# Kernel optimization log

Measured on AMD Instinct MI355X. Metric: run time of the kernel, lower is better.

The kernel has to match this reference:

```python
import jax, jax.numpy as jnp
import numpy as np

HIDDEN = 1024
FFN = 4 * HIDDEN
NUM_EXPERTS = 8
TOP_K = 2
B, S = 4, 2048


def setup_inputs() -> dict:
    key = jax.random.key(0)
    ks = jax.random.split(key, 7)
    scale = 0.02
    return {
        "x": jax.random.normal(ks[0], (B, S, HIDDEN), dtype=jnp.float32),
        "gate_w": jax.random.normal(ks[1], (HIDDEN, NUM_EXPERTS), dtype=jnp.float32) * scale,
        "gate_b": jnp.zeros((NUM_EXPERTS,), dtype=jnp.float32),
        "w1": jax.random.normal(ks[2], (NUM_EXPERTS, HIDDEN, FFN), dtype=jnp.float32) * scale,
        "b1": jnp.zeros((NUM_EXPERTS, FFN), dtype=jnp.float32),
        "w2": jax.random.normal(ks[3], (NUM_EXPERTS, FFN, HIDDEN), dtype=jnp.float32) * scale,
        "b2": jnp.zeros((NUM_EXPERTS, HIDDEN), dtype=jnp.float32),
    }


def reference(x, gate_w, gate_b, w1, b1, w2, b2):
    b, s, h = x.shape
    xt = x.reshape(b * s, h)  # [T, H]
    # gate: Linear + softmax
    probs = jax.nn.softmax(xt @ gate_w + gate_b, axis=-1)  # [T, E]
    _, idx = jax.lax.top_k(probs, TOP_K)  # [T, K] int32
    # one-hot over top-k -> boolean per-expert mask (matches original one_hot.sum>0)
    one_hot = jax.nn.one_hot(idx, NUM_EXPERTS, dtype=xt.dtype)  # [T, K, E]
    mask = (one_hot.sum(axis=1) > 0).astype(xt.dtype)  # [T, E]
    # every expert MLP applied to all tokens (dense equivalent of gather-MLP-scatter),
    # then masked combine: output[t] = sum_e mask[t,e] * MLP_e(x[t])
    h1 = jax.nn.relu(jnp.einsum('th,ehf->etf', xt, w1) + b1[:, None, :])  # [E, T, F]
    out_e = jnp.einsum('etf,efh->eth', h1, w2) + b2[:, None, :]  # [E, T, H]
    out = jnp.einsum('eth,te->th', out_e, mask)  # [T, H]
    return out.reshape(b, s, h)
```

## Files before the change

kernel.cpp:

```cpp
#include <hip/hip_runtime.h>

typedef __bf16 bf16_t;
typedef bf16_t bf16x8 __attribute__((ext_vector_type(8)));
typedef bf16_t bf16x4 __attribute__((ext_vector_type(4)));
typedef float floatx4 __attribute__((ext_vector_type(4)));

#define T_TOKENS 8192
#define HIDDEN 1024
#define FFN 4096
#define NE 8
#define PAIRS 16384
#define NTILES 136
#define BK 64

#define GLD16(gp, lp) __builtin_amdgcn_global_load_lds( \
    (const __attribute__((address_space(1))) void*)(gp), \
    (__attribute__((address_space(3))) void*)(lp), 16, 0, 0)

__global__ __launch_bounds__(256) void gate_kernel(
    const float* __restrict__ x, const float* __restrict__ gw,
    const float* __restrict__ gb, unsigned* __restrict__ top2,
    int* __restrict__ counts, bf16_t* __restrict__ xb)
{
    const int lane = threadIdx.x & 63;
    const int wid  = threadIdx.x >> 6;
    const int t    = blockIdx.x * 4 + wid;
    const float4* xr = (const float4*)(x + (size_t)t * HIDDEN);
    bf16_t* xo = xb + (size_t)t * HIDDEN;

    float s[NE];
#pragma unroll
    for (int e = 0; e < NE; ++e) s[e] = 0.f;
#pragma unroll
    for (int ii = 0; ii < 4; ++ii) {
        const int i = ii * 64 + lane;
        float4 v = xr[i];
        bf16x4 b;
        b[0] = (bf16_t)v.x; b[1] = (bf16_t)v.y; b[2] = (bf16_t)v.z; b[3] = (bf16_t)v.w;
        *(bf16x4*)(xo + i * 4) = b;
        const float* g = gw + (size_t)i * 32;
#pragma unroll
        for (int j = 0; j < 4; ++j) {
            const float xv = (&v.x)[j];
#pragma unroll
            for (int e = 0; e < NE; ++e) s[e] += xv * g[j * 8 + e];
        }
    }
#pragma unroll
    for (int e = 0; e < NE; ++e) {
#pragma unroll
        for (int off = 32; off > 0; off >>= 1) s[e] += __shfl_xor(s[e], off, 64);
    }
    if (lane == 0) {
        float v1 = -1e30f, v2 = -1e30f;
        int i1 = 0, i2 = 0;
#pragma unroll
        for (int e = 0; e < NE; ++e) {
            float v = s[e] + gb[e];
            if (v > v1)      { v2 = v1; i2 = i1; v1 = v; i1 = e; }
            else if (v > v2) { v2 = v;  i2 = e; }
        }
        top2[t] = (unsigned)(i1 | (i2 << 4));
        atomicAdd(&counts[i1], 1);
        atomicAdd(&counts[i2], 1);
    }
}

__global__ void offsets_kernel(const int* __restrict__ counts,
                               int* __restrict__ offs,
                               int* __restrict__ tinfo)
{
    int acc = 0, nt = 0;
    for (int e = 0; e < NE; ++e) {
        offs[e] = acc;
        int n = counts[e];
        for (int r = 0; r < n; r += 128) tinfo[nt++] = e | ((r >> 7) << 4);
        acc += n;
    }
    for (; nt < NTILES; ++nt) tinfo[nt] = (65535 << 4);
}

__global__ __launch_bounds__(256) void scatter_kernel(
    const unsigned* __restrict__ top2, const int* __restrict__ offs,
    int* __restrict__ fill, unsigned short* __restrict__ tok16)
{
    const int t = blockIdx.x * 256 + threadIdx.x;
    const unsigned v = top2[t];
    const int e1 = v & 15, e2 = (v >> 4) & 15;
    tok16[offs[e1] + atomicAdd(&fill[e1], 1)] = (unsigned short)t;
    tok16[offs[e2] + atomicAdd(&fill[e2], 1)] = (unsigned short)t;
}

__global__ __launch_bounds__(256) void wtrans_kernel(
    const float* __restrict__ in, bf16_t* __restrict__ out, int R, int C)
{
    __shared__ bf16_t L[64][68];
    const int e  = blockIdx.z;
    const int r0 = blockIdx.y * 64;
    const int c0 = blockIdx.x * 64;
    const float* ip = in + ((size_t)e * R + r0) * C + c0;
    bf16_t* op = out + ((size_t)e * C + c0) * R + r0;
    const int tid = threadIdx.x;
    const int lr = tid >> 4, lc4 = tid & 15;
#pragma unroll
    for (int p = 0; p < 4; ++p) {
        int r = p * 16 + lr;
        float4 v = *(const float4*)(ip + (size_t)r * C + lc4 * 4);
        bf16x4 b;
        b[0] = (bf16_t)v.x; b[1] = (bf16_t)v.y; b[2] = (bf16_t)v.z; b[3] = (bf16_t)v.w;
        *(bf16x4*)&L[r][lc4 * 4] = b;
    }
    __syncthreads();
#pragma unroll
    for (int p = 0; p < 4; ++p) {
        int c  = p * 16 + lr;
        int rr = lc4 * 4;
        bf16x4 b;
        b[0] = L[rr + 0][c]; b[1] = L[rr + 1][c];
        b[2] = L[rr + 2][c]; b[3] = L[rr + 3][c];
        *(bf16x4*)(op + (size_t)c * R + rr) = b;
    }
}

__global__ __launch_bounds__(256, 3) void moe_gemm1(
    const bf16_t* __restrict__ xb, const bf16_t* __restrict__ w1t,
    const float* __restrict__ b1, const int* __restrict__ counts,
    const int* __restrict__ offs, const unsigned short* __restrict__ tok16,
    const int* __restrict__ tinfo, bf16_t* __restrict__ h1)
{
    const int nx = gridDim.x;
    const int hw = blockIdx.y * nx + blockIdx.x;
    const int chunk = (nx * gridDim.y) >> 3;
    const int l  = (hw & 7) * chunk + (hw >> 3);
    const int bx = l % nx;
    const int by = l / nx;

    const int info = tinfo[by];
    const int e    = info & 15;
    const int row0 = (info >> 4) << 7;
    const int n_e  = counts[e];
    if (row0 >= n_e) return;
    const int seg   = offs[e];
    const int fcol0 = bx * 128;

    __shared__ bf16_t S[128 * 128];
    bf16_t* As = S;
    bf16_t* Bs = S + 128 * BK;

    const int tid  = threadIdx.x;
    const int wid  = tid >> 6, lane = tid & 63;
    const int wm   = wid & 1,  wn   = wid >> 1;
    const int quad = lane >> 4, lrow = lane & 15;

    const bf16_t* pA[4]; const bf16_t* pB[4];
#pragma unroll
    for (int q = 0; q < 4; ++q) {
        int slot = q * 256 + tid;
        int arow = slot >> 3, ko = slot & 7;
        int kos  = ko ^ (arow & 7);
        int ridx = row0 + arow; if (ridx > n_e - 1) ridx = n_e - 1;
        pA[q] = xb + (size_t)tok16[seg + ridx] * HIDDEN + kos * 8;
        pB[q] = w1t + ((size_t)e * FFN + fcol0 + arow) * HIDDEN + kos * 8;
    }

    floatx4 acc[4][4];
#pragma unroll
    for (int i = 0; i < 4; ++i)
#pragma unroll
        for (int j = 0; j < 4; ++j) acc[i][j] = (floatx4){0.f, 0.f, 0.f, 0.f};

    for (int k0 = 0; k0 < HIDDEN; k0 += BK) {
#pragma unroll
        for (int q = 0; q < 4; ++q) {
            GLD16(pA[q], As + (q * 256 + wid * 64) * 8);
            GLD16(pB[q], Bs + (q * 256 + wid * 64) * 8);
            pA[q] += BK; pB[q] += BK;
        }
        __syncthreads();
#pragma unroll
        for (int h = 0; h < 2; ++h) {
            bf16x8 af[4], bfr[4];
#pragma unroll
            for (int mi = 0; mi < 4; ++mi) {
                int r = wm * 64 + mi * 16 + lrow;
                int g = (h * 4 + quad) ^ (r & 7);
                af[mi] = *(const bf16x8*)&As[(r << 6) + (g << 3)];
            }
#pragma unroll
            for (int ni = 0; ni < 4; ++ni) {
                int r = wn * 64 + ni * 16 + lrow;
                int g = (h * 4 + quad) ^ (r & 7);
                bfr[ni] = *(const bf16x8*)&Bs[(r << 6) + (g << 3)];
            }
#pragma unroll
            for (int mi = 0; mi < 4; ++mi)
#pragma unroll
                for (int ni = 0; ni < 4; ++ni)
                    acc[mi][ni] = __builtin_amdgcn_mfma_f32_16x16x32_bf16(
                        af[mi], bfr[ni], acc[mi][ni], 0, 0, 0);
        }
        __syncthreads();
    }

#pragma unroll
    for (int ni = 0; ni < 4; ++ni) {
        const int col = wn * 64 + ni * 16 + lrow;
        const float bias = b1[(size_t)e * FFN + fcol0 + col];
#pragma unroll
        for (int mi = 0; mi < 4; ++mi)
#pragma unroll
            for (int r = 0; r < 4; ++r) {
                int row = wm * 64 + mi * 16 + quad * 4 + r;
                float v = acc[mi][ni][r] + bias;
                v = v > 0.f ? v : 0.f;
                S[row * 128 + col] = (bf16_t)v;
            }
    }
    __syncthreads();
#pragma unroll
    for (int i = 0; i < 8; ++i) {
        int g16 = i * 256 + tid;
        int row = g16 >> 4;
        int ce  = (g16 & 15) * 8;
        if (row0 + row < n_e)
            *(bf16x8*)(h1 + (size_t)(seg + row0 + row) * FFN + fcol0 + ce) =
                *(const bf16x8*)&S[row * 128 + ce];
    }
}

__global__ __launch_bounds__(256, 3) void moe_gemm2(
    const bf16_t* __restrict__ h1, const bf16_t* __restrict__ w2t,
    const float* __restrict__ b2, const int* __restrict__ counts,
    const int* __restrict__ offs, const unsigned short* __restrict__ tok16,
    const int* __restrict__ tinfo, float* __restrict__ out)
{
    const int nx = gridDim.x;
    const int hw = blockIdx.y * nx + blockIdx.x;
    const int chunk = (nx * gridDim.y) >> 3;
    const int l  = (hw & 7) * chunk + (hw >> 3);
    const int bx = l % nx;
    const int by = l / nx;

    const int info = tinfo[by];
    const int e    = info & 15;
    const int row0 = (info >> 4) << 7;
    const int n_e  = counts[e];
    if (row0 >= n_e) return;
    const int seg   = offs[e];
    const int hcol0 = bx * 128;

    __shared__ bf16_t As[128 * BK];
    __shared__ bf16_t Bs[128 * BK];

    const int tid  = threadIdx.x;
    const int wid  = tid >> 6, lane = tid & 63;
    const int wm   = wid & 1,  wn   = wid >> 1;
    const int quad = lane >> 4, lrow = lane & 15;

    const bf16_t* pA[4]; const bf16_t* pB[4];
#pragma unroll
    for (int q = 0; q < 4; ++q) {
        int slot = q * 256 + tid;
        int arow = slot >> 3, ko = slot & 7;
        int kos  = ko ^ (arow & 7);
        int ridx = row0 + arow; if (ridx > n_e - 1) ridx = n_e - 1;
        pA[q] = h1 + (size_t)(seg + ridx) * FFN + kos * 8;
        pB[q] = w2t + ((size_t)e * HIDDEN + hcol0 + arow) * FFN + kos * 8;
    }

    floatx4 acc[4][4];
#pragma unroll
    for (int i = 0; i < 4; ++i)
#pragma unroll
        for (int j = 0; j < 4; ++j) acc[i][j] = (floatx4){0.f, 0.f, 0.f, 0.f};

    for (int k0 = 0; k0 < FFN; k0 += BK) {
#pragma unroll
        for (int q = 0; q < 4; ++q) {
            GLD16(pA[q], As + (q * 256 + wid * 64) * 8);
            GLD16(pB[q], Bs + (q * 256 + wid * 64) * 8);
            pA[q] += BK; pB[q] += BK;
        }
        __syncthreads();
#pragma unroll
        for (int h = 0; h < 2; ++h) {
            bf16x8 af[4], bfr[4];
#pragma unroll
            for (int mi = 0; mi < 4; ++mi) {
                int r = wm * 64 + mi * 16 + lrow;
                int g = (h * 4 + quad) ^ (r & 7);
                af[mi] = *(const bf16x8*)&As[(r << 6) + (g << 3)];
            }
#pragma unroll
            for (int ni = 0; ni < 4; ++ni) {
                int r = wn * 64 + ni * 16 + lrow;
                int g = (h * 4 + quad) ^ (r & 7);
                bfr[ni] = *(const bf16x8*)&Bs[(r << 6) + (g << 3)];
            }
#pragma unroll
            for (int mi = 0; mi < 4; ++mi)
#pragma unroll
                for (int ni = 0; ni < 4; ++ni)
                    acc[mi][ni] = __builtin_amdgcn_mfma_f32_16x16x32_bf16(
                        af[mi], bfr[ni], acc[mi][ni], 0, 0, 0);
        }
        __syncthreads();
    }

    int tokr[4][4];
#pragma unroll
    for (int mi = 0; mi < 4; ++mi)
#pragma unroll
        for (int r = 0; r < 4; ++r) {
            int row = wm * 64 + mi * 16 + quad * 4 + r;
            tokr[mi][r] = (row0 + row < n_e) ? (int)tok16[seg + row0 + row] : -1;
        }
#pragma unroll
    for (int ni = 0; ni < 4; ++ni) {
        const int col = wn * 64 + ni * 16 + lrow;
        const float bias = b2[(size_t)e * HIDDEN + hcol0 + col];
#pragma unroll
        for (int mi = 0; mi < 4; ++mi)
#pragma unroll
            for (int r = 0; r < 4; ++r) {
                if (tokr[mi][r] >= 0)
                    atomicAdd(out + (size_t)tokr[mi][r] * HIDDEN + hcol0 + col,
                              acc[mi][ni][r] + bias);
            }
    }
}

extern "C" void kernel_launch(void* const* d_in, const int* in_sizes, int n_in,
                              void* d_out, int out_size, void* d_ws, size_t ws_size,
                              hipStream_t stream)
{
    const float* x      = (const float*)d_in[0];
    const float* gate_w = (const float*)d_in[1];
    const float* gate_b = (const float*)d_in[2];
    const float* w1     = (const float*)d_in[3];
    const float* b1     = (const float*)d_in[4];
    const float* w2     = (const float*)d_in[5];
    const float* b2     = (const float*)d_in[6];
    float* out = (float*)d_out;

    char* ws = (char*)d_ws;
    int*      counts = (int*)(ws + 0);
    int*      fill   = (int*)(ws + 32);
    int*      offs   = (int*)(ws + 64);
    int*      tinfo  = (int*)(ws + 96);
    unsigned* top2   = (unsigned*)(ws + 640);
    unsigned short* tok16 = (unsigned short*)(ws + 640 + 32768);
    const size_t o_base = 98560;

    const size_t sz_xb  = (size_t)T_TOKENS * HIDDEN * 2;
    const size_t sz_w1t = (size_t)NE * FFN * HIDDEN * 2;
    const size_t sz_w2t = (size_t)NE * HIDDEN * FFN * 2;
    const size_t sz_h1  = (size_t)PAIRS * FFN * 2;
    const size_t need = o_base + sz_xb + sz_w1t + sz_w2t + sz_h1;
    if (ws_size < need) return;

    bf16_t* xb  = (bf16_t*)(ws + o_base);
    bf16_t* w1t = (bf16_t*)(ws + o_base + sz_xb);
    bf16_t* w2t = (bf16_t*)(ws + o_base + sz_xb + sz_w1t);
    bf16_t* h1  = (bf16_t*)(ws + o_base + sz_xb + sz_w1t + sz_w2t);

    hipMemsetAsync(ws, 0, 96, stream);
    hipMemsetAsync(out, 0, (size_t)T_TOKENS * HIDDEN * sizeof(float), stream);

    gate_kernel<<<T_TOKENS / 4, 256, 0, stream>>>(x, gate_w, gate_b, top2, counts, xb);
    offsets_kernel<<<1, 1, 0, stream>>>(counts, offs, tinfo);
    scatter_kernel<<<T_TOKENS / 256, 256, 0, stream>>>(top2, offs, fill, tok16);

    wtrans_kernel<<<dim3(FFN / 64, HIDDEN / 64, NE), 256, 0, stream>>>(w1, w1t, HIDDEN, FFN);
    wtrans_kernel<<<dim3(HIDDEN / 64, FFN / 64, NE), 256, 0, stream>>>(w2, w2t, FFN, HIDDEN);

    moe_gemm1<<<dim3(FFN / 128, NTILES), 256, 0, stream>>>(
        xb, w1t, b1, counts, offs, tok16, tinfo, h1);
    moe_gemm2<<<dim3(HIDDEN / 128, NTILES), 256, 0, stream>>>(
        h1, w2t, b2, counts, offs, tok16, tinfo, out);
}
```

Measured before the change: 1.013 ms.

## Double-buffer LDS tiles in MoE GEMMs with async prefetch overlap

Both expert GEMM kernels now use two LDS stages so that the next K-tile's global-to-LDS loads are issued before computing on the current tile, with explicit vmcnt waits and raw barriers instead of full syncthreads. MFMA sections are wrapped in s_setprio to favor math waves. The goal is to hide global memory latency behind the matrix math. LDS use doubles to 64KB per block and occupancy bounds drop from 3 to 2 blocks per CU, which could reduce latency hiding across blocks.

After: 1.033 ms. Within noise of the previous version (+2.0%).

```diff
diff --git a/kernel.cpp b/kernel.cpp
--- a/kernel.cpp
+++ b/kernel.cpp
@@ -16,6 +16,15 @@
 #define GLD16(gp, lp) __builtin_amdgcn_global_load_lds( \
     (const __attribute__((address_space(1))) void*)(gp), \
     (__attribute__((address_space(3))) void*)(lp), 16, 0, 0)
+
+#define STAGE8(DA, DB) do { \
+    _Pragma("unroll") \
+    for (int q = 0; q < 4; ++q) { \
+        GLD16(pA[q], (DA) + (q * 256 + wid * 64) * 8); \
+        GLD16(pB[q], (DB) + (q * 256 + wid * 64) * 8); \
+        pA[q] += BK; pB[q] += BK; \
+    } \
+} while (0)
 
 __global__ __launch_bounds__(256) void gate_kernel(
     const float* __restrict__ x, const float* __restrict__ gw,
@@ -122,7 +131,7 @@
     }
 }
 
-__global__ __launch_bounds__(256, 3) void moe_gemm1(
+__global__ __launch_bounds__(256, 2) void moe_gemm1(
     const bf16_t* __restrict__ xb, const bf16_t* __restrict__ w1t,
     const float* __restrict__ b1, const int* __restrict__ counts,
     const int* __restrict__ offs, const unsigned short* __restrict__ tok16,
@@ -143,9 +152,11 @@
     const int seg   = offs[e];
     const int fcol0 = bx * 128;
 
-    __shared__ bf16_t S[128 * 128];
-    bf16_t* As = S;
-    bf16_t* Bs = S + 128 * BK;
+    __shared__ bf16_t S[4 * 128 * BK];
+    bf16_t* As0 = S;
+    bf16_t* Bs0 = S + 128 * BK;
+    bf16_t* As1 = S + 2 * 128 * BK;
+    bf16_t* Bs1 = S + 3 * 128 * BK;
 
     const int tid  = threadIdx.x;
     const int wid  = tid >> 6, lane = tid & 63;
@@ -169,14 +180,7 @@
 #pragma unroll
         for (int j = 0; j < 4; ++j) acc[i][j] = (floatx4){0.f, 0.f, 0.f, 0.f};
 
-    for (int k0 = 0; k0 < HIDDEN; k0 += BK) {
-#pragma unroll
-        for (int q = 0; q < 4; ++q) {
-            GLD16(pA[q], As + (q * 256 + wid * 64) * 8);
-            GLD16(pB[q], Bs + (q * 256 + wid * 64) * 8);
-            pA[q] += BK; pB[q] += BK;
-        }
-        __syncthreads();
+    auto compute = [&](const bf16_t* AS, const bf16_t* BS) {
 #pragma unroll
         for (int h = 0; h < 2; ++h) {
             bf16x8 af[4], bfr[4];
@@ -184,23 +188,46 @@
             for (int mi = 0; mi < 4; ++mi) {
                 int r = wm * 64 + mi * 16 + lrow;
                 int g = (h * 4 + quad) ^ (r & 7);
-                af[mi] = *(const bf16x8*)&As[(r << 6) + (g << 3)];
+                af[mi] = *(const bf16x8*)&AS[(r << 6) + (g << 3)];
             }
 #pragma unroll
             for (int ni = 0; ni < 4; ++ni) {
                 int r = wn * 64 + ni * 16 + lrow;
                 int g = (h * 4 + quad) ^ (r & 7);
-                bfr[ni] = *(const bf16x8*)&Bs[(r << 6) + (g << 3)];
-            }
+                bfr[ni] = *(const bf16x8*)&BS[(r << 6) + (g << 3)];
+            }
+            __builtin_amdgcn_s_setprio(1);
 #pragma unroll
             for (int mi = 0; mi < 4; ++mi)
 #pragma unroll
                 for (int ni = 0; ni < 4; ++ni)
                     acc[mi][ni] = __builtin_amdgcn_mfma_f32_16x16x32_bf16(
                         af[mi], bfr[ni], acc[mi][ni], 0, 0, 0);
+            __builtin_amdgcn_s_setprio(0);
         }
-        __syncthreads();
-    }
+    };
+
+    STAGE8(As0, Bs0);
+    bf16_t* curA = As0; bf16_t* curB = Bs0;
+    bf16_t* nxtA = As1; bf16_t* nxtB = Bs1;
+
+    const int NK = HIDDEN / BK;
+#pragma unroll 2
+    for (int kt = 1; kt < NK; ++kt) {
+        STAGE8(nxtA, nxtB);
+        asm volatile("s_waitcnt vmcnt(8)" ::: "memory");
+        __builtin_amdgcn_s_barrier();
+        asm volatile("" ::: "memory");
+        compute(curA, curB);
+        asm volatile("s_waitcnt lgkmcnt(0)" ::: "memory");
+        __builtin_amdgcn_s_barrier();
+        bf16_t* tA = curA; curA = nxtA; nxtA = tA;
+        bf16_t* tB = curB; curB = nxtB; nxtB = tB;
+    }
+    asm volatile("s_waitcnt vmcnt(0)" ::: "memory");
+    __builtin_amdgcn_s_barrier();
+    asm volatile("" ::: "memory");
+    compute(curA, curB);
 
 #pragma unroll
     for (int ni = 0; ni < 4; ++ni) {
@@ -228,7 +255,7 @@
     }
 }
 
-__global__ __launch_bounds__(256, 3) void moe_gemm2(
+__global__ __launch_bounds__(256, 2) void moe_gemm2(
     const bf16_t* __restrict__ h1, const bf16_t* __restrict__ w2t,
     const float* __restrict__ b2, const int* __restrict__ counts,
     const int* __restrict__ offs, const unsigned short* __restrict__ tok16,
@@ -249,8 +276,11 @@
     const int seg   = offs[e];
     const int hcol0 = bx * 128;
 
-    __shared__ bf16_t As[128 * BK];
-    __shared__ bf16_t Bs[128 * BK];
+    __shared__ bf16_t S[4 * 128 * BK];
+    bf16_t* As0 = S;
+    bf16_t* Bs0 = S + 128 * BK;
+    bf16_t* As1 = S + 2 * 128 * BK;
+    bf16_t* Bs1 = S + 3 * 128 * BK;
 
     const int tid  = threadIdx.x;
     const int wid  = tid >> 6, lane = tid & 63;
@@ -274,14 +304,7 @@
 #pragma unroll
         for (int j = 0; j < 4; ++j) acc[i][j] = (floatx4){0.f, 0.f, 0.f, 0.f};
 
-    for (int k0 = 0; k0 < FFN; k0 += BK) {
-#pragma unroll
-        for (int q = 0; q < 4; ++q) {
-            GLD16(pA[q], As + (q * 256 + wid * 64) * 8);
-            GLD16(pB[q], Bs + (q * 256 + wid * 64) * 8);
-            pA[q] += BK; pB[q] += BK;
-        }
-        __syncthreads();
+    auto compute = [&](const bf16_t* AS, const bf16_t* BS) {
 #pragma unroll
         for (int h = 0; h < 2; ++h) {
             bf16x8 af[4], bfr[4];
@@ -289,23 +312,46 @@
             for (int mi = 0; mi < 4; ++mi) {
                 int r = wm * 64 + mi * 16 + lrow;
                 int g = (h * 4 + quad) ^ (r & 7);
-                af[mi] = *(const bf16x8*)&As[(r << 6) + (g << 3)];
+                af[mi] = *(const bf16x8*)&AS[(r << 6) + (g << 3)];
             }
 #pragma unroll
             for (int ni = 0; ni < 4; ++ni) {
                 int r = wn * 64 + ni * 16 + lrow;
                 int g = (h * 4 + quad) ^ (r & 7);
-                bfr[ni] = *(const bf16x8*)&Bs[(r << 6) + (g << 3)];
-            }
+                bfr[ni] = *(const bf16x8*)&BS[(r << 6) + (g << 3)];
+            }
+            __builtin_amdgcn_s_setprio(1);
 #pragma unroll
             for (int mi = 0; mi < 4; ++mi)
 #pragma unroll
                 for (int ni = 0; ni < 4; ++ni)
                     acc[mi][ni] = __builtin_amdgcn_mfma_f32_16x16x32_bf16(
                         af[mi], bfr[ni], acc[mi][ni], 0, 0, 0);
+            __builtin_amdgcn_s_setprio(0);
         }
-        __syncthreads();
-    }
+    };
+
+    STAGE8(As0, Bs0);
+    bf16_t* curA = As0; bf16_t* curB = Bs0;
+    bf16_t* nxtA = As1; bf16_t* nxtB = Bs1;
+
+    const int NK = FFN / BK;
+#pragma unroll 2
+    for (int kt = 1; kt < NK; ++kt) {
+        STAGE8(nxtA, nxtB);
+        asm volatile("s_waitcnt vmcnt(8)" ::: "memory");
+        __builtin_amdgcn_s_barrier();
+        asm volatile("" ::: "memory");
+        compute(curA, curB);
+        asm volatile("s_waitcnt lgkmcnt(0)" ::: "memory");
+        __builtin_amdgcn_s_barrier();
+        bf16_t* tA = curA; curA = nxtA; nxtA = tA;
+        bf16_t* tB = curB; curB = nxtB; nxtB = tB;
+    }
+    asm volatile("s_waitcnt vmcnt(0)" ::: "memory");
+    __builtin_amdgcn_s_barrier();
+    asm volatile("" ::: "memory");
+    compute(curA, curB);
 
     int tokr[4][4];
 #pragma unroll
```

## Use 256x256 tiles with double-buffered pipelined MFMA GEMMs and split-K GEMM2

Applied to the files above, without the earlier changes.

Both expert GEMMs move from 128x128 tiles with 256 threads to 256x256 tiles with 512 threads. They use a 128KB double-buffered LDS ring with async global-to-LDS loads interleaved between MFMA phases, explicit waitcnt/barrier scheduling, and setprio. GEMM2 also splits K in two halves so the smaller grid still fills the device, relying on the existing atomic accumulation. The intent is to raise arithmetic intensity and hide load latency behind compute. The cost is higher register and LDS pressure, more atomics, and padding waste on partial 256-row tiles.

Result: slower. 1.068 ms (+5.4%).

```diff
diff --git a/kernel.cpp b/kernel.cpp
--- a/kernel.cpp
+++ b/kernel.cpp
@@ -10,12 +10,86 @@
 #define FFN 4096
 #define NE 8
 #define PAIRS 16384
-#define NTILES 136
+#define NT256 72
 #define BK 64
 
 #define GLD16(gp, lp) __builtin_amdgcn_global_load_lds( \
     (const __attribute__((address_space(1))) void*)(gp), \
     (__attribute__((address_space(3))) void*)(lp), 16, 0, 0)
+
+#define ST_A(b, h, t_) do { \
+    const size_t tb_ = (size_t)(((t_) < NKT) ? (t_) : (NKT - 1)) * 128; \
+    GLD16(baseA + (size_t)voffA[(h)*2+0] + tb_, \
+          SH + (b)*16384 + ((h)*128 +  0 + w8)*64); \
+    GLD16(baseA + (size_t)voffA[(h)*2+1] + tb_, \
+          SH + (b)*16384 + ((h)*128 + 64 + w8)*64); \
+} while (0)
+#define ST_B(b, h, t_) do { \
+    const size_t tb_ = (size_t)(((t_) < NKT) ? (t_) : (NKT - 1)) * 128; \
+    GLD16(baseB + (size_t)voffB[(h)*2+0] + tb_, \
+          SH + 32768 + (b)*16384 + ((h)*128 +  0 + w8)*64); \
+    GLD16(baseB + (size_t)voffB[(h)*2+1] + tb_, \
+          SH + 32768 + (b)*16384 + ((h)*128 + 64 + w8)*64); \
+} while (0)
+
+#define RDA(mi, h, coff) af[mi][h] = *(const bf16x8*)(SH + (coff) + \
+    (wm*128 + (mi)*16 + lrow)*64 + ((((h)<<2)|quad) ^ lsw)*8)
+#define RDB(ni, h, coff) bfr[ni][h] = *(const bf16x8*)(SH + 32768 + (coff) + \
+    (wn*64 + (ni)*16 + lrow)*64 + ((((h)<<2)|quad) ^ lsw)*8)
+
+#define MM1(mi, ni, h) acc[mi][ni] = __builtin_amdgcn_mfma_f32_16x16x32_bf16( \
+    af[mi][h], bfr[ni][h], acc[mi][ni], 0, 0, 0)
+#define MM4x2(mb, nb) do { \
+    MM1(mb+0, nb+0, 0); MM1(mb+0, nb+1, 0); MM1(mb+1, nb+0, 0); MM1(mb+1, nb+1, 0); \
+    MM1(mb+2, nb+0, 0); MM1(mb+2, nb+1, 0); MM1(mb+3, nb+0, 0); MM1(mb+3, nb+1, 0); \
+    MM1(mb+0, nb+0, 1); MM1(mb+0, nb+1, 1); MM1(mb+1, nb+0, 1); MM1(mb+1, nb+1, 1); \
+    MM1(mb+2, nb+0, 1); MM1(mb+2, nb+1, 1); MM1(mb+3, nb+0, 1); MM1(mb+3, nb+1, 1); \
+} while (0)
+
+#define TILE_PHASES(t_, cur, nxt) do { \
+    asm volatile("s_waitcnt vmcnt(6)" ::: "memory"); \
+    __builtin_amdgcn_s_barrier(); \
+    asm volatile("" ::: "memory"); \
+    { const int coff = (cur)*16384; \
+      RDA(0,0,coff); RDA(0,1,coff); RDA(1,0,coff); RDA(1,1,coff); \
+      RDA(2,0,coff); RDA(2,1,coff); RDA(3,0,coff); RDA(3,1,coff); \
+      RDB(0,0,coff); RDB(0,1,coff); RDB(1,0,coff); RDB(1,1,coff); \
+      RDB(2,0,coff); RDB(2,1,coff); RDB(3,0,coff); RDB(3,1,coff); } \
+    ST_A(nxt, 1, (t_)+1); \
+    asm volatile("s_waitcnt lgkmcnt(0)" ::: "memory"); \
+    __builtin_amdgcn_sched_barrier(0); \
+    __builtin_amdgcn_s_setprio(1); \
+    MM4x2(0, 0); \
+    __builtin_amdgcn_s_setprio(0); \
+    __builtin_amdgcn_s_barrier(); \
+    asm volatile("" ::: "memory"); \
+    { const int coff = (cur)*16384; \
+      RDA(4,0,coff); RDA(4,1,coff); RDA(5,0,coff); RDA(5,1,coff); \
+      RDA(6,0,coff); RDA(6,1,coff); RDA(7,0,coff); RDA(7,1,coff); } \
+    ST_B(cur, 0, (t_)+2); \
+    asm volatile("s_waitcnt lgkmcnt(0)" ::: "memory"); \
+    __builtin_amdgcn_sched_barrier(0); \
+    __builtin_amdgcn_s_setprio(1); \
+    MM4x2(0, 2); \
+    __builtin_amdgcn_s_setprio(0); \
+    __builtin_amdgcn_s_barrier(); \
+    asm volatile("" ::: "memory"); \
+    ST_A(cur, 0, (t_)+2); \
+    ST_B(cur, 1, (t_)+2); \
+    __builtin_amdgcn_s_setprio(1); \
+    MM4x2(4, 0); MM4x2(4, 2); \
+    __builtin_amdgcn_s_setprio(0); \
+} while (0)
+
+#define GEMM_GEOM() \
+    const int tid  = threadIdx.x; \
+    const int wid  = tid >> 6, lane = tid & 63; \
+    const int wm   = wid >> 2, wn   = wid & 3; \
+    const int quad = lane >> 4, lrow = lane & 15; \
+    const int lsw  = lrow & 7; \
+    const int w8   = wid * 8; \
+    const int row8 = tid >> 3; \
+    const int gs   = (tid & 7) ^ (row8 & 7)
 
 __global__ __launch_bounds__(256) void gate_kernel(
     const float* __restrict__ x, const float* __restrict__ gw,
@@ -74,10 +148,10 @@
     for (int e = 0; e < NE; ++e) {
         offs[e] = acc;
         int n = counts[e];
-        for (int r = 0; r < n; r += 128) tinfo[nt++] = e | ((r >> 7) << 4);
+        for (int r = 0; r < n; r += 256) tinfo[nt++] = e | ((r >> 8) << 4);
         acc += n;
     }
-    for (; nt < NTILES; ++nt) tinfo[nt] = (65535 << 4);
+    for (; nt < NT256; ++nt) tinfo[nt] = (65535 << 4);
 }
 
 __global__ __launch_bounds__(256) void scatter_kernel(
@@ -122,12 +196,15 @@
     }
 }
 
-__global__ __launch_bounds__(256, 3) void moe_gemm1(
+__global__ __launch_bounds__(512, 2) void moe_gemm1(
     const bf16_t* __restrict__ xb, const bf16_t* __restrict__ w1t,
     const float* __restrict__ b1, const int* __restrict__ counts,
     const int* __restrict__ offs, const unsigned short* __restrict__ tok16,
     const int* __restrict__ tinfo, bf16_t* __restrict__ h1)
 {
+    __shared__ __align__(16) bf16_t SH[65536];
+    const int NKT = HIDDEN / BK;
+
     const int nx = gridDim.x;
     const int hw = blockIdx.y * nx + blockIdx.x;
     const int chunk = (nx * gridDim.y) >> 3;
@@ -137,103 +214,80 @@
 
     const int info = tinfo[by];
     const int e    = info & 15;
-    const int row0 = (info >> 4) << 7;
+    const int row0 = (info >> 4) << 8;
     const int n_e  = counts[e];
     if (row0 >= n_e) return;
     const int seg   = offs[e];
-    const int fcol0 = bx * 128;
-
-    __shared__ bf16_t S[128 * 128];
-    bf16_t* As = S;
-    bf16_t* Bs = S + 128 * BK;
-
-    const int tid  = threadIdx.x;
-    const int wid  = tid >> 6, lane = tid & 63;
-    const int wm   = wid & 1,  wn   = wid >> 1;
-    const int quad = lane >> 4, lrow = lane & 15;
-
-    const bf16_t* pA[4]; const bf16_t* pB[4];
-#pragma unroll
-    for (int q = 0; q < 4; ++q) {
-        int slot = q * 256 + tid;
-        int arow = slot >> 3, ko = slot & 7;
-        int kos  = ko ^ (arow & 7);
-        int ridx = row0 + arow; if (ridx > n_e - 1) ridx = n_e - 1;
-        pA[q] = xb + (size_t)tok16[seg + ridx] * HIDDEN + kos * 8;
-        pB[q] = w1t + ((size_t)e * FFN + fcol0 + arow) * HIDDEN + kos * 8;
-    }
-
-    floatx4 acc[4][4];
-#pragma unroll
-    for (int i = 0; i < 4; ++i)
+    const int fcol0 = bx * 256;
+
+    GEMM_GEOM();
+
+    unsigned voffA[4], voffB[4];
+#pragma unroll
+    for (int j = 0; j < 4; ++j) {
+        int rj = j * 64 + row8;
+        int ridx = row0 + rj; if (ridx > n_e - 1) ridx = n_e - 1;
+        voffA[j] = (unsigned)tok16[seg + ridx] * (HIDDEN * 2) + gs * 16;
+        voffB[j] = (unsigned)(fcol0 + rj) * (HIDDEN * 2) + gs * 16;
+    }
+    const char* baseA = (const char*)xb;
+    const char* baseB = (const char*)w1t + (size_t)e * FFN * HIDDEN * 2;
+
+    floatx4 acc[8][4];
+#pragma unroll
+    for (int i = 0; i < 8; ++i)
 #pragma unroll
         for (int j = 0; j < 4; ++j) acc[i][j] = (floatx4){0.f, 0.f, 0.f, 0.f};
-
-    for (int k0 = 0; k0 < HIDDEN; k0 += BK) {
-#pragma unroll
-        for (int q = 0; q < 4; ++q) {
-            GLD16(pA[q], As + (q * 256 + wid * 64) * 8);
-            GLD16(pB[q], Bs + (q * 256 + wid * 64) * 8);
-            pA[q] += BK; pB[q] += BK;
+    bf16x8 af[8][2], bfr[4][2];
+
+    ST_B(0, 0, 0); ST_A(0, 0, 0); ST_B(0, 1, 0); ST_A(0, 1, 0);
+    ST_B(1, 0, 1); ST_A(1, 0, 1); ST_B(1, 1, 1);
+
+    for (int t = 0; t < NKT; t += 2) {
+        TILE_PHASES(t,     0, 1);
+        TILE_PHASES(t + 1, 1, 0);
+    }
+
+    asm volatile("s_waitcnt vmcnt(0)" ::: "memory");
+    __builtin_amdgcn_s_barrier();
+    asm volatile("" ::: "memory");
+    const float* b1g = b1 + (size_t)e * FFN + fcol0;
+    float bias[4];
+#pragma unroll
+    for (int ni = 0; ni < 4; ++ni) bias[ni] = b1g[wn * 64 + ni * 16 + lrow];
+#pragma unroll
+    for (int mi = 0; mi < 8; ++mi)
+#pragma unroll
+        for (int ni = 0; ni < 4; ++ni) {
+            const int col = wn * 64 + ni * 16 + lrow;
+#pragma unroll
+            for (int r = 0; r < 4; ++r) {
+                int row = wm * 128 + mi * 16 + quad * 4 + r;
+                float v = acc[mi][ni][r] + bias[ni];
+                v = v > 0.f ? v : 0.f;
+                SH[row * 256 + (col ^ ((row & 7) << 3))] = (bf16_t)v;
+            }
         }
-        __syncthreads();
-#pragma unroll
-        for (int h = 0; h < 2; ++h) {
-            bf16x8 af[4], bfr[4];
-#pragma unroll
-            for (int mi = 0; mi < 4; ++mi) {
-                int r = wm * 64 + mi * 16 + lrow;
-                int g = (h * 4 + quad) ^ (r & 7);
-                af[mi] = *(const bf16x8*)&As[(r << 6) + (g << 3)];
-            }
-#pragma unroll
-            for (int ni = 0; ni < 4; ++ni) {
-                int r = wn * 64 + ni * 16 + lrow;
-                int g = (h * 4 + quad) ^ (r & 7);
-                bfr[ni] = *(const bf16x8*)&Bs[(r << 6) + (g << 3)];
-            }
-#pragma unroll
-            for (int mi = 0; mi < 4; ++mi)
-#pragma unroll
-                for (int ni = 0; ni < 4; ++ni)
-                    acc[mi][ni] = __builtin_amdgcn_mfma_f32_16x16x32_bf16(
-                        af[mi], bfr[ni], acc[mi][ni], 0, 0, 0);
-        }
-        __syncthreads();
-    }
-
-#pragma unroll
-    for (int ni = 0; ni < 4; ++ni) {
-        const int col = wn * 64 + ni * 16 + lrow;
-        const float bias = b1[(size_t)e * FFN + fcol0 + col];
-#pragma unroll
-        for (int mi = 0; mi < 4; ++mi)
-#pragma unroll
-            for (int r = 0; r < 4; ++r) {
-                int row = wm * 64 + mi * 16 + quad * 4 + r;
-                float v = acc[mi][ni][r] + bias;
-                v = v > 0.f ? v : 0.f;
-                S[row * 128 + col] = (bf16_t)v;
-            }
-    }
     __syncthreads();
 #pragma unroll
-    for (int i = 0; i < 8; ++i) {
-        int g16 = i * 256 + tid;
-        int row = g16 >> 4;
-        int ce  = (g16 & 15) * 8;
+    for (int i = 0; i < 16; ++i) {
+        int gidx = i * 512 + tid;
+        int row = gidx >> 5, g = gidx & 31;
         if (row0 + row < n_e)
-            *(bf16x8*)(h1 + (size_t)(seg + row0 + row) * FFN + fcol0 + ce) =
-                *(const bf16x8*)&S[row * 128 + ce];
-    }
-}
-
-__global__ __launch_bounds__(256, 3) void moe_gemm2(
+            *(bf16x8*)(h1 + (size_t)(seg + row0 + row) * FFN + fcol0 + g * 8) =
+                *(const bf16x8*)(SH + row * 256 + ((g * 8) ^ ((row & 7) << 3)));
+    }
+}
+
+__global__ __launch_bounds__(512, 2) void moe_gemm2(
     const bf16_t* __restrict__ h1, const bf16_t* __restrict__ w2t,
     const float* __restrict__ b2, const int* __restrict__ counts,
     const int* __restrict__ offs, const unsigned short* __restrict__ tok16,
     const int* __restrict__ tinfo, float* __restrict__ out)
 {
+    __shared__ __align__(16) bf16_t SH[65536];
+    const int NKT = (FFN / 2) / BK;
+
     const int nx = gridDim.x;
     const int hw = blockIdx.y * nx + blockIdx.x;
     const int chunk = (nx * gridDim.y) >> 3;
@@ -243,91 +297,63 @@
 
     const int info = tinfo[by];
     const int e    = info & 15;
-    const int row0 = (info >> 4) << 7;
+    const int row0 = (info >> 4) << 8;
     const int n_e  = counts[e];
     if (row0 >= n_e) return;
     const int seg   = offs[e];
-    const int hcol0 = bx * 128;
-
-    __shared__ bf16_t As[128 * BK];
-    __shared__ bf16_t Bs[128 * BK];
-
-    const int tid  = threadIdx.x;
-    const int wid  = tid >> 6, lane = tid & 63;
-    const int wm   = wid & 1,  wn   = wid >> 1;
-    const int quad = lane >> 4, lrow = lane & 15;
-
-    const bf16_t* pA[4]; const bf16_t* pB[4];
-#pragma unroll
-    for (int q = 0; q < 4; ++q) {
-        int slot = q * 256 + tid;
-        int arow = slot >> 3, ko = slot & 7;
-        int kos  = ko ^ (arow & 7);
-        int ridx = row0 + arow; if (ridx > n_e - 1) ridx = n_e - 1;
-        pA[q] = h1 + (size_t)(seg + ridx) * FFN + kos * 8;
-        pB[q] = w2t + ((size_t)e * HIDDEN + hcol0 + arow) * FFN + kos * 8;
-    }
-
-    floatx4 acc[4][4];
-#pragma unroll
-    for (int i = 0; i < 4; ++i)
+    const int hcol0 = (bx & 3) * 256;
+    const int kh    = bx >> 2;
+
+    GEMM_GEOM();
+
+    unsigned voffA[4], voffB[4];
+#pragma unroll
+    for (int j = 0; j < 4; ++j) {
+        int rj = j * 64 + row8;
+        int ridx = row0 + rj; if (ridx > n_e - 1) ridx = n_e - 1;
+        voffA[j] = (unsigned)(seg + ridx) * (FFN * 2) + gs * 16;
+        voffB[j] = (unsigned)(hcol0 + rj) * (FFN * 2) + gs * 16;
+    }
+    const char* baseA = (const char*)h1 + (size_t)kh * (FFN / 2) * 2;
+    const char* baseB = (const char*)w2t + (size_t)e * HIDDEN * FFN * 2
+                        + (size_t)kh * (FFN / 2) * 2;
+
+    floatx4 acc[8][4];
+#pragma unroll
+    for (int i = 0; i < 8; ++i)
 #pragma unroll
         for (int j = 0; j < 4; ++j) acc[i][j] = (floatx4){0.f, 0.f, 0.f, 0.f};
-
-    for (int k0 = 0; k0 < FFN; k0 += BK) {
-#pragma unroll
-        for (int q = 0; q < 4; ++q) {
-            GLD16(pA[q], As + (q * 256 + wid * 64) * 8);
-            GLD16(pB[q], Bs + (q * 256 + wid * 64) * 8);
-            pA[q] += BK; pB[q] += BK;
+    bf16x8 af[8][2], bfr[4][2];
+
+    ST_B(0, 0, 0); ST_A(0, 0, 0); ST_B(0, 1, 0); ST_A(0, 1, 0);
+    ST_B(1, 0, 1); ST_A(1, 0, 1); ST_B(1, 1, 1);
+
+    for (int t = 0; t < NKT; t += 2) {
+        TILE_PHASES(t,     0, 1);
+        TILE_PHASES(t + 1, 1, 0);
+    }
+
+    asm volatile("s_waitcnt vmcnt(0)" ::: "memory");
+
+    const float* b2g = b2 + (size_t)e * HIDDEN + hcol0;
+    float bias[4];
+#pragma unroll
+    for (int ni = 0; ni < 4; ++ni)
+        bias[ni] = (kh == 0) ? b2g[wn * 64 + ni * 16 + lrow] : 0.f;
+#pragma unroll
+    for (int mi = 0; mi < 8; ++mi)
+#pragma unroll
+        for (int r = 0; r < 4; ++r) {
+            int row = wm * 128 + mi * 16 + quad * 4 + r;
+            if (row0 + row < n_e) {
+                int tok = tok16[seg + row0 + row];
+                float* op = out + (size_t)tok * HIDDEN + hcol0;
+#pragma unroll
+                for (int ni = 0; ni < 4; ++ni)
+                    atomicAdd(op + wn * 64 + ni * 16 + lrow,
+                              acc[mi][ni][r] + bias[ni]);
+            }
         }
-        __syncthreads();
-#pragma unroll
-        for (int h = 0; h < 2; ++h) {
-            bf16x8 af[4], bfr[4];
-#pragma unroll
-            for (int mi = 0; mi < 4; ++mi) {
-                int r = wm * 64 + mi * 16 + lrow;
-                int g = (h * 4 + quad) ^ (r & 7);
-                af[mi] = *(const bf16x8*)&As[(r << 6) + (g << 3)];
-            }
-#pragma unroll
-            for (int ni = 0; ni < 4; ++ni) {
-                int r = wn * 64 + ni * 16 + lrow;
-                int g = (h * 4 + quad) ^ (r & 7);
-                bfr[ni] = *(const bf16x8*)&Bs[(r << 6) + (g << 3)];
-            }
-#pragma unroll
-            for (int mi = 0; mi < 4; ++mi)
-#pragma unroll
-                for (int ni = 0; ni < 4; ++ni)
-                    acc[mi][ni] = __builtin_amdgcn_mfma_f32_16x16x32_bf16(
-                        af[mi], bfr[ni], acc[mi][ni], 0, 0, 0);
-        }
-        __syncthreads();
-    }
-
-    int tokr[4][4];
-#pragma unroll
-    for (int mi = 0; mi < 4; ++mi)
-#pragma unroll
-        for (int r = 0; r < 4; ++r) {
-            int row = wm * 64 + mi * 16 + quad * 4 + r;
-            tokr[mi][r] = (row0 + row < n_e) ? (int)tok16[seg + row0 + row] : -1;
-        }
-#pragma unroll
-    for (int ni = 0; ni < 4; ++ni) {
-        const int col = wn * 64 + ni * 16 + lrow;
-        const float bias = b2[(size_t)e * HIDDEN + hcol0 + col];
-#pragma unroll
-        for (int mi = 0; mi < 4; ++mi)
-#pragma unroll
-            for (int r = 0; r < 4; ++r) {
-                if (tokr[mi][r] >= 0)
-                    atomicAdd(out + (size_t)tokr[mi][r] * HIDDEN + hcol0 + col,
-                              acc[mi][ni][r] + bias);
-            }
-    }
 }
 
 extern "C" void kernel_launch(void* const* d_in, const int* in_sizes, int n_in,
@@ -374,8 +400,8 @@
     wtrans_kernel<<<dim3(FFN / 64, HIDDEN / 64, NE), 256, 0, stream>>>(w1, w1t, HIDDEN, FFN);
     wtrans_kernel<<<dim3(HIDDEN / 64, FFN / 64, NE), 256, 0, stream>>>(w2, w2t, FFN, HIDDEN);
 
-    moe_gemm1<<<dim3(FFN / 128, NTILES), 256, 0, stream>>>(
+    moe_gemm1<<<dim3(FFN / 256, NT256), 512, 0, stream>>>(
         xb, w1t, b1, counts, offs, tok16, tinfo, h1);
-    moe_gemm2<<<dim3(HIDDEN / 128, NTILES), 256, 0, stream>>>(
+    moe_gemm2<<<dim3((HIDDEN / 256) * 2, NT256), 512, 0, stream>>>(
         h1, w2t, b2, counts, offs, tok16, tinfo, out);
 }
```

## Triple-buffer grouped GEMM K-loop with async LDS prefetch and merge weight transposes

Applied to the files above, without the earlier changes.

Replaces the single-buffered K loop in both expert GEMMs with a three-stage LDS ring (BK=32). The next-but-one tile is prefetched via global_load_lds while MFMAs run, with a single barrier per step, vmcnt waits and setprio around the MFMA block. The aim is to hide global-load latency and remove the second sync per iteration. It also fuses the two weight-transpose launches into one and pads the epilogue LDS stride to reduce bank conflicts. Risks include a halved K per barrier, more LDS per block (48KB), which may reduce occupancy, and fragile hand-written waitcnt logic.

New measurement: 1.057 ms. 4.3% more time.

```diff
diff --git a/kernel.cpp b/kernel.cpp
--- a/kernel.cpp
+++ b/kernel.cpp
@@ -11,11 +11,50 @@
 #define NE 8
 #define PAIRS 16384
 #define NTILES 136
-#define BK 64
+#define BK 32
 
 #define GLD16(gp, lp) __builtin_amdgcn_global_load_lds( \
     (const __attribute__((address_space(1))) void*)(gp), \
     (__attribute__((address_space(3))) void*)(lp), 16, 0, 0)
+
+#define STAGE(bb, t_) do { \
+    const size_t tb_ = (size_t)(((t_) < NKT) ? (t_) : (NKT - 1)) * (BK * 2); \
+    GLD16(baseA + (size_t)voffA0 + tb_, SH + (bb) + (wid * 64) * 8); \
+    GLD16(baseA + (size_t)voffA1 + tb_, SH + (bb) + (256 + wid * 64) * 8); \
+    GLD16(baseB + (size_t)voffB0 + tb_, SH + (bb) + 4096 + (wid * 64) * 8); \
+    GLD16(baseB + (size_t)voffB1 + tb_, SH + (bb) + 4096 + (256 + wid * 64) * 8); \
+} while (0)
+
+#define KSTEP(t_, cb, sb) do { \
+    asm volatile("s_waitcnt vmcnt(4)" ::: "memory"); \
+    __builtin_amdgcn_s_barrier(); \
+    asm volatile("" ::: "memory"); \
+    bf16x8 af[4], bfr[4]; \
+    _Pragma("unroll") \
+    for (int mi = 0; mi < 4; ++mi) \
+        af[mi] = *(const bf16x8*)&SH[(cb) + (wm * 64 + mi * 16 + lrow) * 32 + kx8]; \
+    _Pragma("unroll") \
+    for (int ni = 0; ni < 4; ++ni) \
+        bfr[ni] = *(const bf16x8*)&SH[(cb) + 4096 + (wn * 64 + ni * 16 + lrow) * 32 + kx8]; \
+    STAGE(sb, (t_) + 2); \
+    asm volatile("s_waitcnt lgkmcnt(0)" ::: "memory"); \
+    __builtin_amdgcn_sched_barrier(0); \
+    __builtin_amdgcn_s_setprio(1); \
+    _Pragma("unroll") \
+    for (int mi = 0; mi < 4; ++mi) \
+        _Pragma("unroll") \
+        for (int ni = 0; ni < 4; ++ni) \
+            acc[mi][ni] = __builtin_amdgcn_mfma_f32_16x16x32_bf16( \
+                af[mi], bfr[ni], acc[mi][ni], 0, 0, 0); \
+    __builtin_amdgcn_s_setprio(0); \
+} while (0)
+
+#define GEMM_GEOM() \
+    const int tid  = threadIdx.x; \
+    const int wid  = tid >> 6, lane = tid & 63; \
+    const int wm   = wid & 1,  wn   = wid >> 1; \
+    const int quad = lane >> 4, lrow = lane & 15; \
+    const int kx8  = ((quad ^ (lrow & 3)) << 3)
 
 __global__ __launch_bounds__(256) void gate_kernel(
     const float* __restrict__ x, const float* __restrict__ gw,
@@ -92,12 +131,21 @@
 }
 
 __global__ __launch_bounds__(256) void wtrans_kernel(
-    const float* __restrict__ in, bf16_t* __restrict__ out, int R, int C)
+    const float* __restrict__ w1, bf16_t* __restrict__ w1t,
+    const float* __restrict__ w2, bf16_t* __restrict__ w2t)
 {
     __shared__ bf16_t L[64][68];
-    const int e  = blockIdx.z;
-    const int r0 = blockIdx.y * 64;
-    const int c0 = blockIdx.x * 64;
+    const int bid = blockIdx.x;
+    const int sel = bid >> 13;
+    const int e   = (bid & 8191) >> 10;
+    const int tl  = bid & 1023;
+    const int R = sel ? FFN : HIDDEN;
+    const int C = sel ? HIDDEN : FFN;
+    const int cx = sel ? (tl & 15) : (tl & 63);
+    const int ry = sel ? (tl >> 4) : (tl >> 6);
+    const float* in = (sel ? w2 : w1);
+    bf16_t* out = (sel ? w2t : w1t);
+    const int r0 = ry * 64, c0 = cx * 64;
     const float* ip = in + ((size_t)e * R + r0) * C + c0;
     bf16_t* op = out + ((size_t)e * C + c0) * R + r0;
     const int tid = threadIdx.x;
@@ -128,6 +176,9 @@
     const int* __restrict__ offs, const unsigned short* __restrict__ tok16,
     const int* __restrict__ tinfo, bf16_t* __restrict__ h1)
 {
+    __shared__ __align__(16) bf16_t SH[24576];
+    const int NKT = HIDDEN / BK;
+
     const int nx = gridDim.x;
     const int hw = blockIdx.y * nx + blockIdx.x;
     const int chunk = (nx * gridDim.y) >> 3;
@@ -143,25 +194,22 @@
     const int seg   = offs[e];
     const int fcol0 = bx * 128;
 
-    __shared__ bf16_t S[128 * 128];
-    bf16_t* As = S;
-    bf16_t* Bs = S + 128 * BK;
-
-    const int tid  = threadIdx.x;
-    const int wid  = tid >> 6, lane = tid & 63;
-    const int wm   = wid & 1,  wn   = wid >> 1;
-    const int quad = lane >> 4, lrow = lane & 15;
-
-    const bf16_t* pA[4]; const bf16_t* pB[4];
-#pragma unroll
-    for (int q = 0; q < 4; ++q) {
-        int slot = q * 256 + tid;
-        int arow = slot >> 3, ko = slot & 7;
-        int kos  = ko ^ (arow & 7);
-        int ridx = row0 + arow; if (ridx > n_e - 1) ridx = n_e - 1;
-        pA[q] = xb + (size_t)tok16[seg + ridx] * HIDDEN + kos * 8;
-        pB[q] = w1t + ((size_t)e * FFN + fcol0 + arow) * HIDDEN + kos * 8;
-    }
+    GEMM_GEOM();
+
+    unsigned voffA0, voffA1, voffB0, voffB1;
+    {
+        int s0 = tid, s1 = 256 + tid;
+        int a0 = s0 >> 2, a1 = s1 >> 2;
+        int g0 = (s0 & 3) ^ (a0 & 3), g1 = (s1 & 3) ^ (a1 & 3);
+        int r0i = row0 + a0; if (r0i > n_e - 1) r0i = n_e - 1;
+        int r1i = row0 + a1; if (r1i > n_e - 1) r1i = n_e - 1;
+        voffA0 = (unsigned)tok16[seg + r0i] * (HIDDEN * 2) + g0 * 16;
+        voffA1 = (unsigned)tok16[seg + r1i] * (HIDDEN * 2) + g1 * 16;
+        voffB0 = (unsigned)(fcol0 + a0) * (HIDDEN * 2) + g0 * 16;
+        voffB1 = (unsigned)(fcol0 + a1) * (HIDDEN * 2) + g1 * 16;
+    }
+    const char* baseA = (const char*)xb;
+    const char* baseB = (const char*)w1t + (size_t)e * FFN * HIDDEN * 2;
 
     floatx4 acc[4][4];
 #pragma unroll
@@ -169,51 +217,33 @@
 #pragma unroll
         for (int j = 0; j < 4; ++j) acc[i][j] = (floatx4){0.f, 0.f, 0.f, 0.f};
 
-    for (int k0 = 0; k0 < HIDDEN; k0 += BK) {
-#pragma unroll
-        for (int q = 0; q < 4; ++q) {
-            GLD16(pA[q], As + (q * 256 + wid * 64) * 8);
-            GLD16(pB[q], Bs + (q * 256 + wid * 64) * 8);
-            pA[q] += BK; pB[q] += BK;
-        }
-        __syncthreads();
-#pragma unroll
-        for (int h = 0; h < 2; ++h) {
-            bf16x8 af[4], bfr[4];
-#pragma unroll
-            for (int mi = 0; mi < 4; ++mi) {
-                int r = wm * 64 + mi * 16 + lrow;
-                int g = (h * 4 + quad) ^ (r & 7);
-                af[mi] = *(const bf16x8*)&As[(r << 6) + (g << 3)];
-            }
-#pragma unroll
-            for (int ni = 0; ni < 4; ++ni) {
-                int r = wn * 64 + ni * 16 + lrow;
-                int g = (h * 4 + quad) ^ (r & 7);
-                bfr[ni] = *(const bf16x8*)&Bs[(r << 6) + (g << 3)];
-            }
-#pragma unroll
-            for (int mi = 0; mi < 4; ++mi)
-#pragma unroll
-                for (int ni = 0; ni < 4; ++ni)
-                    acc[mi][ni] = __builtin_amdgcn_mfma_f32_16x16x32_bf16(
-                        af[mi], bfr[ni], acc[mi][ni], 0, 0, 0);
-        }
-        __syncthreads();
-    }
-
+    STAGE(0, 0);
+    STAGE(8192, 1);
+    int cb = 0, sb = 16384;
+    for (int t = 0; t < NKT; ++t) {
+        KSTEP(t, cb, sb);
+        cb = (cb == 16384) ? 0 : cb + 8192;
+        sb = (sb == 16384) ? 0 : sb + 8192;
+    }
+
+    asm volatile("s_waitcnt vmcnt(0)" ::: "memory");
+    __builtin_amdgcn_s_barrier();
+    asm volatile("" ::: "memory");
+    const float* b1g = b1 + (size_t)e * FFN + fcol0;
+    float bias[4];
+#pragma unroll
+    for (int ni = 0; ni < 4; ++ni) bias[ni] = b1g[wn * 64 + ni * 16 + lrow];
 #pragma unroll
     for (int ni = 0; ni < 4; ++ni) {
         const int col = wn * 64 + ni * 16 + lrow;
-        const float bias = b1[(size_t)e * FFN + fcol0 + col];
 #pragma unroll
         for (int mi = 0; mi < 4; ++mi)
 #pragma unroll
             for (int r = 0; r < 4; ++r) {
                 int row = wm * 64 + mi * 16 + quad * 4 + r;
-                float v = acc[mi][ni][r] + bias;
+                float v = acc[mi][ni][r] + bias[ni];
                 v = v > 0.f ? v : 0.f;
-                S[row * 128 + col] = (bf16_t)v;
+                SH[row * 136 + col] = (bf16_t)v;
             }
     }
     __syncthreads();
@@ -224,7 +254,7 @@
         int ce  = (g16 & 15) * 8;
         if (row0 + row < n_e)
             *(bf16x8*)(h1 + (size_t)(seg + row0 + row) * FFN + fcol0 + ce) =
-                *(const bf16x8*)&S[row * 128 + ce];
+                *(const bf16x8*)&SH[row * 136 + ce];
     }
 }
 
@@ -234,6 +264,9 @@
     const int* __restrict__ offs, const unsigned short* __restrict__ tok16,
     const int* __restrict__ tinfo, float* __restrict__ out)
 {
+    __shared__ __align__(16) bf16_t SH[24576];
+    const int NKT = FFN / BK;
+
     const int nx = gridDim.x;
     const int hw = blockIdx.y * nx + blockIdx.x;
     const int chunk = (nx * gridDim.y) >> 3;
@@ -249,24 +282,22 @@
     const int seg   = offs[e];
     const int hcol0 = bx * 128;
 
-    __shared__ bf16_t As[128 * BK];
-    __shared__ bf16_t Bs[128 * BK];
-
-    const int tid  = threadIdx.x;
-    const int wid  = tid >> 6, lane = tid & 63;
-    const int wm   = wid & 1,  wn   = wid >> 1;
-    const int quad = lane >> 4, lrow = lane & 15;
-
-    const bf16_t* pA[4]; const bf16_t* pB[4];
-#pragma unroll
-    for (int q = 0; q < 4; ++q) {
-        int slot = q * 256 + tid;
-        int arow = slot >> 3, ko = slot & 7;
-        int kos  = ko ^ (arow & 7);
-        int ridx = row0 + arow; if (ridx > n_e - 1) ridx = n_e - 1;
-        pA[q] = h1 + (size_t)(seg + ridx) * FFN + kos * 8;
-        pB[q] = w2t + ((size_t)e * HIDDEN + hcol0 + arow) * FFN + kos * 8;
-    }
+    GEMM_GEOM();
+
+    unsigned voffA0, voffA1, voffB0, voffB1;
+    {
+        int s0 = tid, s1 = 256 + tid;
+        int a0 = s0 >> 2, a1 = s1 >> 2;
+        int g0 = (s0 & 3) ^ (a0 & 3), g1 = (s1 & 3) ^ (a1 & 3);
+        int r0i = row0 + a0; if (r0i > n_e - 1) r0i = n_e - 1;
+        int r1i = row0 + a1; if (r1i > n_e - 1) r1i = n_e - 1;
+        voffA0 = (unsigned)(seg + r0i) * (FFN * 2) + g0 * 16;
+        voffA1 = (unsigned)(seg + r1i) * (FFN * 2) + g1 * 16;
+        voffB0 = (unsigned)(hcol0 + a0) * (FFN * 2) + g0 * 16;
+        voffB1 = (unsigned)(hcol0 + a1) * (FFN * 2) + g1 * 16;
+    }
+    const char* baseA = (const char*)h1;
+    const char* baseB = (const char*)w2t + (size_t)e * HIDDEN * FFN * 2;
 
     floatx4 acc[4][4];
 #pragma unroll
@@ -274,38 +305,16 @@
 #pragma unroll
         for (int j = 0; j < 4; ++j) acc[i][j] = (floatx4){0.f, 0.f, 0.f, 0.f};
 
-    for (int k0 = 0; k0 < FFN; k0 += BK) {
-#pragma unroll
-        for (int q = 0; q < 4; ++q) {
-            GLD16(pA[q], As + (q * 256 + wid * 64) * 8);
-            GLD16(pB[q], Bs + (q * 256 + wid * 64) * 8);
-            pA[q] += BK; pB[q] += BK;
-        }
-        __syncthreads();
-#pragma unroll
-        for (int h = 0; h < 2; ++h) {
-            bf16x8 af[4], bfr[4];
-#pragma unroll
-            for (int mi = 0; mi < 4; ++mi) {
-                int r = wm * 64 + mi * 16 + lrow;
-                int g = (h * 4 + quad) ^ (r & 7);
-                af[mi] = *(const bf16x8*)&As[(r << 6) + (g << 3)];
-            }
-#pragma unroll
-            for (int ni = 0; ni < 4; ++ni) {
-                int r = wn * 64 + ni * 16 + lrow;
-                int g = (h * 4 + quad) ^ (r & 7);
-                bfr[ni] = *(const bf16x8*)&Bs[(r << 6) + (g << 3)];
-            }
-#pragma unroll
-            for (int mi = 0; mi < 4; ++mi)
-#pragma unroll
-                for (int ni = 0; ni < 4; ++ni)
-                    acc[mi][ni] = __builtin_amdgcn_mfma_f32_16x16x32_bf16(
-                        af[mi], bfr[ni], acc[mi][ni], 0, 0, 0);
-        }
-        __syncthreads();
-    }
+    STAGE(0, 0);
+    STAGE(8192, 1);
+    int cb = 0, sb = 16384;
+    for (int t = 0; t < NKT; ++t) {
+        KSTEP(t, cb, sb);
+        cb = (cb == 16384) ? 0 : cb + 8192;
+        sb = (sb == 16384) ? 0 : sb + 8192;
+    }
+
+    asm volatile("s_waitcnt vmcnt(0)" ::: "memory");
 
     int tokr[4][4];
 #pragma unroll
@@ -371,8 +380,7 @@
     offsets_kernel<<<1, 1, 0, stream>>>(counts, offs, tinfo);
     scatter_kernel<<<T_TOKENS / 256, 256, 0, stream>>>(top2, offs, fill, tok16);
 
-    wtrans_kernel<<<dim3(FFN / 64, HIDDEN / 64, NE), 256, 0, stream>>>(w1, w1t, HIDDEN, FFN);
-    wtrans_kernel<<<dim3(HIDDEN / 64, FFN / 64, NE), 256, 0, stream>>>(w2, w2t, FFN, HIDDEN);
+    wtrans_kernel<<<16384, 256, 0, stream>>>(w1, w1t, w2, w2t);
 
     moe_gemm1<<<dim3(FFN / 128, NTILES), 256, 0, stream>>>(
         xb, w1t, b1, counts, offs, tok16, tinfo, h1);
```
